# Kernel tuning notes

Hardware: AMD Instinct MI355X
Metric: run time of the kernel (lower is better)

Reference implementation:

```python
import jax, jax.numpy as jnp
import numpy as np

B, L, D, H = 2, 2048, 1024, 16
HD = D // H
SCALE = HD ** -0.5


def setup_inputs() -> dict:
    key = jax.random.key(0)
    ks = jax.random.split(key, 11)
    s = D ** -0.5  # torch Linear default init scale (uniform bound)
    return {
        "q": jax.random.normal(ks[0], (B, L, D), jnp.float32),
        "k": jax.random.normal(ks[1], (B, L, D), jnp.float32),
        "v": jax.random.normal(ks[2], (B, L, D), jnp.float32),
        "Wq": jax.random.uniform(ks[3], (D, D), jnp.float32, -s, s),
        "bq": jax.random.uniform(ks[4], (D,), jnp.float32, -s, s),
        "Wk": jax.random.uniform(ks[5], (D, D), jnp.float32, -s, s),
        "bk": jax.random.uniform(ks[6], (D,), jnp.float32, -s, s),
        "Wv": jax.random.uniform(ks[7], (D, D), jnp.float32, -s, s),
        "bv": jax.random.uniform(ks[8], (D,), jnp.float32, -s, s),
        "Wo": jax.random.uniform(ks[9], (D, D), jnp.float32, -s, s),
        "bo": jax.random.uniform(ks[10], (D,), jnp.float32, -s, s),
    }


def reference(q, k, v, Wq, bq, Wk, bk, Wv, bv, Wo, bo):
    b, q_len, _ = q.shape
    # projections; weights stored as (D, D) acting on the right: x @ W + b
    qh = (q @ Wq + bq).reshape(b, q_len, H, HD).transpose(0, 2, 1, 3)  # (B,H,Q,hd)
    kh = (k @ Wk + bk).reshape(b, -1, H, HD).transpose(0, 2, 1, 3)    # (B,H,K,hd)
    vh = (v @ Wv + bv).reshape(b, -1, H, HD).transpose(0, 2, 1, 3)    # (B,H,K,hd)
    att = jnp.einsum("bhqd,bhkd->bhqk", qh * SCALE, kh)               # (B,H,Q,K)
    att = jax.nn.softmax(att, axis=-1)
    out = jnp.einsum("bhqk,bhkd->bhqd", att, vh)                      # (B,H,Q,hd)
    out = out.transpose(0, 2, 1, 3).reshape(b, q_len, D)
    return out @ Wo + bo
```

## Files before the change

### kernel.cpp

```cpp
#include <hip/hip_runtime.h>

namespace {
constexpr int kB  = 2;
constexpr int kL  = 2048;
constexpr int kD  = 1024;
constexpr int kH  = 16;
constexpr int kHD = 64;
constexpr int kM  = kB * kL;
}

typedef _Float16 f16x8 __attribute__((ext_vector_type(8)));
typedef float    f32x16 __attribute__((ext_vector_type(16)));
typedef unsigned int u32;

union Frag16 { uint4 u4; unsigned u[4]; f16x8 v; };

__device__ __forceinline__ unsigned short f2h(float f) {
    return __builtin_bit_cast(unsigned short, (_Float16)f);
}
__device__ __forceinline__ unsigned pk2(float a, float b) {
    return __builtin_bit_cast(unsigned, __builtin_amdgcn_cvt_pkrtz(a, b));
}
__device__ __forceinline__ float max3f(float a, float b, float c) {
    float d;
    asm("v_max3_f32 %0, %1, %2, %3" : "=v"(d) : "v"(a), "v"(b), "v"(c));
    return d;
}

__device__ __forceinline__ void gload16(const void* g, void* l) {
    __builtin_amdgcn_global_load_lds(
        (const __attribute__((address_space(1))) u32*)g,
        (__attribute__((address_space(3))) u32*)(unsigned long long)(__builtin_bit_cast(unsigned long long, l)),
        16, 0, 0);
}

__global__ __launch_bounds__(256) void cast_f16_kernel(
    const float* __restrict__ q, const float* __restrict__ k,
    const float* __restrict__ v, unsigned short* __restrict__ dst)
{
    const float* src = blockIdx.y == 0 ? q : (blockIdx.y == 1 ? k : v);
    unsigned short* d = dst + (size_t)blockIdx.y * ((size_t)kM * kD);
    const size_t i = ((size_t)blockIdx.x * 256 + threadIdx.x) * 8;
    const float4 f0 = *(const float4*)(src + i);
    const float4 f1 = *(const float4*)(src + i + 4);
    _Float16 h[8];
    h[0] = (_Float16)f0.x; h[1] = (_Float16)f0.y;
    h[2] = (_Float16)f0.z; h[3] = (_Float16)f0.w;
    h[4] = (_Float16)f1.x; h[5] = (_Float16)f1.y;
    h[6] = (_Float16)f1.z; h[7] = (_Float16)f1.w;
    *(uint4*)(d + i) = *(uint4*)h;
}

__global__ __launch_bounds__(256) void tcast_kernel(
    const float* __restrict__ W0, const float* __restrict__ W1,
    const float* __restrict__ W2, const float* __restrict__ W3,
    unsigned short* __restrict__ WtBase)
{
    __shared__ _Float16 T[64][68];
    const float* W = blockIdx.z == 0 ? W0 : blockIdx.z == 1 ? W1
                   : blockIdx.z == 2 ? W2 : W3;
    unsigned short* Wt = WtBase + (size_t)blockIdx.z * ((size_t)kD * kD);
    const int k0 = blockIdx.y * 64, n0 = blockIdx.x * 64;
    const int tx = threadIdx.x & 15, ty = threadIdx.x >> 4;
#pragma unroll
    for (int i = 0; i < 4; ++i) {
        const int kk = i * 16 + ty;
        const float4 w = *(const float4*)&W[(size_t)(k0 + kk) * kD + n0 + tx * 4];
        T[tx * 4 + 0][kk] = (_Float16)w.x;
        T[tx * 4 + 1][kk] = (_Float16)w.y;
        T[tx * 4 + 2][kk] = (_Float16)w.z;
        T[tx * 4 + 3][kk] = (_Float16)w.w;
    }
    __syncthreads();
#pragma unroll
    for (int i = 0; i < 4; ++i) {
        const int nn = i * 16 + ty;
        *(ushort4*)&Wt[(size_t)(n0 + nn) * kD + k0 + tx * 4] = *(ushort4*)&T[nn][tx * 4];
    }
}

template <int MODE>
__global__ __launch_bounds__(256) void gemm16_kernel(
    const unsigned short* __restrict__ A, const unsigned short* __restrict__ Wt,
    const float* __restrict__ bias, void* __restrict__ Cv)
{
    __shared__ unsigned short Als[2][128 * 64];
    __shared__ unsigned short Bls[2][128 * 64];

    const int tid = threadIdx.x;
    const int lane = tid & 63;
    const int wid = tid >> 6;
    const int l31 = lane & 31;
    const int hi = lane >> 5;
    const int by = blockIdx.x & 31;
    const int bx = blockIdx.x >> 5;
    const int row0 = by * 128;
    const int col0 = bx * 128;
    const int wr = wid >> 1, wc = wid & 1;

    const int rl = lane >> 3;
    const int sl = lane & 7;
    const int ssrc = (sl ^ rl) * 8;

    const unsigned short* Abase = A + (size_t)(row0 + wid * 32 + rl) * kD + ssrc;
    const unsigned short* Bbase = Wt + (size_t)(col0 + wid * 32 + rl) * kD + ssrc;

    f32x16 acc00{}, acc01{}, acc10{}, acc11{};

    auto stage = [&](int kt, int buf) {
#pragma unroll
        for (int i = 0; i < 4; ++i) {
            gload16(Abase + (size_t)(i * 8) * kD + kt * 64,
                    &Als[buf][(wid * 32 + i * 8) * 64]);
        }
#pragma unroll
        for (int i = 0; i < 4; ++i) {
            gload16(Bbase + (size_t)(i * 8) * kD + kt * 64,
                    &Bls[buf][(wid * 32 + i * 8) * 64]);
        }
    };

    const int ra0 = wr * 64 + l31;
    const int cb0 = wc * 64 + l31;

    stage(0, 0);
    int cur = 0;
    for (int kt = 0; kt < kD / 64; ++kt) {
        __syncthreads();
        if (kt + 1 < kD / 64) stage(kt + 1, cur ^ 1);
#pragma unroll
        for (int ks = 0; ks < 4; ++ks) {
            const int slot = (ks << 1) | hi;
            Frag16 a0, a1, b0, b1;
            a0.u4 = *(const uint4*)&Als[cur][ra0 * 64 + ((slot ^ (ra0 & 7)) << 3)];
            a1.u4 = *(const uint4*)&Als[cur][(ra0 + 32) * 64 + ((slot ^ ((ra0 + 32) & 7)) << 3)];
            b0.u4 = *(const uint4*)&Bls[cur][cb0 * 64 + ((slot ^ (cb0 & 7)) << 3)];
            b1.u4 = *(const uint4*)&Bls[cur][(cb0 + 32) * 64 + ((slot ^ ((cb0 + 32) & 7)) << 3)];
            acc00 = __builtin_amdgcn_mfma_f32_32x32x16_f16(a0.v, b0.v, acc00, 0, 0, 0);
            acc01 = __builtin_amdgcn_mfma_f32_32x32x16_f16(a0.v, b1.v, acc01, 0, 0, 0);
            acc10 = __builtin_amdgcn_mfma_f32_32x32x16_f16(a1.v, b0.v, acc10, 0, 0, 0);
            acc11 = __builtin_amdgcn_mfma_f32_32x32x16_f16(a1.v, b1.v, acc11, 0, 0, 0);
        }
        cur ^= 1;
    }

    const float bias0 = bias[col0 + wc * 64 + l31];
    const float bias1 = bias[col0 + wc * 64 + 32 + l31];

    const f32x16* accs[2][2] = {{&acc00, &acc01}, {&acc10, &acc11}};
#pragma unroll
    for (int rt = 0; rt < 2; ++rt) {
#pragma unroll
        for (int ct = 0; ct < 2; ++ct) {
            const f32x16& acv = *accs[rt][ct];
            const float bb = ct ? bias1 : bias0;
            const int c = col0 + wc * 64 + ct * 32 + l31;
            if (MODE == 2) {
                unsigned short* C = (unsigned short*)Cv;
#pragma unroll
                for (int qd = 0; qd < 4; ++qd) {
                    const int r = row0 + wr * 64 + rt * 32 + 8 * qd + 4 * hi;
                    const int b_ = r >> 11, l_ = r & (kL - 1);
                    ushort4 w;
                    w.x = f2h(acv[4 * qd + 0] + bb);
                    w.y = f2h(acv[4 * qd + 1] + bb);
                    w.z = f2h(acv[4 * qd + 2] + bb);
                    w.w = f2h(acv[4 * qd + 3] + bb);
                    *(ushort4*)&C[((size_t)(b_ * kH + (c >> 6)) * kHD + (c & 63)) * kL + l_] = w;
                }
            } else {
#pragma unroll
                for (int reg = 0; reg < 16; ++reg) {
                    const int r = row0 + wr * 64 + rt * 32 + (reg & 3) + 8 * (reg >> 2) + 4 * hi;
                    const float val = acv[reg] + bb;
                    if (MODE == 0) {
                        ((float*)Cv)[(size_t)r * kD + c] = val;
                    } else {
                        const int b_ = r >> 11, l_ = r & (kL - 1);
                        ((unsigned short*)Cv)[((size_t)(b_ * kH + (c >> 6)) * kL + l_) * kHD + (c & 63)] = f2h(val);
                    }
                }
            }
        }
    }
}

__global__ __launch_bounds__(512) void attn_mfma_kernel(
    const unsigned short* __restrict__ Qh, const unsigned short* __restrict__ Kh,
    const unsigned short* __restrict__ Vt, unsigned short* __restrict__ Opart,
    float2* __restrict__ Stat)
{
    __shared__ unsigned short Kls[4][64 * 64];
    __shared__ unsigned short Vls[4][64 * 64];

    const int lane = threadIdx.x & 63;
    const int wid  = threadIdx.x >> 6;
    const int l31  = lane & 31;
    const int hi   = lane >> 5;

    const int id = blockIdx.x;
    const int j  = id >> 3;
    const int bh = (id & 7) * 4 + (j >> 4);
    const int qt = j & 7;
    const int ks = (j >> 3) & 1;
    const int q = qt * 256 + wid * 32 + l31;

    const size_t qkBase = (size_t)bh * kL * kHD;
    const unsigned short* Qp = Qh + qkBase + (size_t)q * kHD + hi * 8;
    Frag16 qf[4];
#pragma unroll
    for (int d = 0; d < 4; ++d) qf[d].u4 = *(const uint4*)(Qp + d * 16);

    const int srow = wid * 8 + (lane >> 3);
    const int soff = (((lane & 7) ^ (srow & 7)) << 3);
    const unsigned short* Kg = Kh + qkBase + (size_t)srow * kHD + soff;
    const unsigned short* Vg = Vt + (size_t)bh * kHD * kL + (size_t)srow * kL + soff;

    auto stage = [&](int kt, int buf) {
        gload16(Kg + (size_t)(kt * 64) * kHD, &Kls[buf][(wid * 8) * 64]);
        gload16(Vg + kt * 64,                 &Vls[buf][(wid * 8) * 64]);
    };

    f16x8 onesv;
#pragma unroll
    for (int i = 0; i < 8; ++i) onesv[i] = (_Float16)1.0f;

    f32x16 o0{}, o1{}, ls{};
    float m = -1e30f;
    const float cexp = 0.125f * 1.44269504089f;

    const int kt0 = ks * 16;
    stage(kt0 + 0, 0);
    stage(kt0 + 1, 1);

    for (int lt = 0; lt < 16; ++lt) {
        if (lt < 15) asm volatile("s_waitcnt vmcnt(2)" ::: "memory");
        else         asm volatile("s_waitcnt vmcnt(0)" ::: "memory");
        __builtin_amdgcn_s_barrier();
        if (lt + 2 < 16) stage(kt0 + lt + 2, (lt + 2) & 3);
        const int cur = lt & 3;

        const int rA = l31, rB = l31 + 32;
        f32x16 c0{}, c1{};
        Frag16 kf0[4], kf1[4];
#pragma unroll
        for (int d = 0; d < 4; ++d) {
            const int s = (d << 1) | hi;
            kf0[d].u4 = *(const uint4*)&Kls[cur][rA * 64 + ((s ^ (rA & 7)) << 3)];
            kf1[d].u4 = *(const uint4*)&Kls[cur][rB * 64 + ((s ^ (rB & 7)) << 3)];
        }
        Frag16 vf0[4], vf1[4];
#pragma unroll
        for (int ksl = 0; ksl < 4; ++ksl) {
            const int s = (ksl << 1) | hi;
            vf0[ksl].u4 = *(const uint4*)&Vls[cur][rA * 64 + ((s ^ (rA & 7)) << 3)];
            vf1[ksl].u4 = *(const uint4*)&Vls[cur][rB * 64 + ((s ^ (rB & 7)) << 3)];
        }
        __builtin_amdgcn_s_setprio(1);
#pragma unroll
        for (int d = 0; d < 4; ++d) {
            c0 = __builtin_amdgcn_mfma_f32_32x32x16_f16(kf0[d].v, qf[d].v, c0, 0, 0, 0);
            c1 = __builtin_amdgcn_mfma_f32_32x32x16_f16(kf1[d].v, qf[d].v, c1, 0, 0, 0);
        }
        __builtin_amdgcn_s_setprio(0);

        float mx = fmaxf(c0[0], c1[0]);
#pragma unroll
        for (int r = 1; r < 16; ++r) mx = max3f(mx, c0[r], c1[r]);
        mx = fmaxf(mx, __shfl_xor(mx, 32));
        if (mx > m + 48.f) {
            const float corr = __builtin_amdgcn_exp2f((m - mx) * cexp);
            m = mx;
            o0 *= corr;
            o1 *= corr;
            ls *= corr;
        }
        const float mc = m * cexp;

        unsigned u0[8], u1[8];
#pragma unroll
        for (int i = 0; i < 8; ++i) {
            u0[i] = pk2(__builtin_amdgcn_exp2f(fmaf(c0[2 * i], cexp, -mc)),
                        __builtin_amdgcn_exp2f(fmaf(c0[2 * i + 1], cexp, -mc)));
            u1[i] = pk2(__builtin_amdgcn_exp2f(fmaf(c1[2 * i], cexp, -mc)),
                        __builtin_amdgcn_exp2f(fmaf(c1[2 * i + 1], cexp, -mc)));
        }
        Frag16 pf[4];
        {
            unsigned t0 = hi ? u0[0] : u0[2];
            unsigned t1 = hi ? u0[1] : u0[3];
            unsigned t2 = hi ? u0[4] : u0[6];
            unsigned t3 = hi ? u0[5] : u0[7];
            const unsigned r0 = __shfl_xor(t0, 32);
            const unsigned r1 = __shfl_xor(t1, 32);
            const unsigned r2 = __shfl_xor(t2, 32);
            const unsigned r3 = __shfl_xor(t3, 32);
            pf[0].u[0] = hi ? r0 : u0[0];
            pf[0].u[1] = hi ? r1 : u0[1];
            pf[0].u[2] = hi ? u0[2] : r0;
            pf[0].u[3] = hi ? u0[3] : r1;
            pf[1].u[0] = hi ? r2 : u0[4];
            pf[1].u[1] = hi ? r3 : u0[5];
            pf[1].u[2] = hi ? u0[6] : r2;
            pf[1].u[3] = hi ? u0[7] : r3;
        }
        {
            unsigned t0 = hi ? u1[0] : u1[2];
            unsigned t1 = hi ? u1[1] : u1[3];
            unsigned t2 = hi ? u1[4] : u1[6];
            unsigned t3 = hi ? u1[5] : u1[7];
            const unsigned r0 = __shfl_xor(t0, 32);
            const unsigned r1 = __shfl_xor(t1, 32);
            const unsigned r2 = __shfl_xor(t2, 32);
            const unsigned r3 = __shfl_xor(t3, 32);
            pf[2].u[0] = hi ? r0 : u1[0];
            pf[2].u[1] = hi ? r1 : u1[1];
            pf[2].u[2] = hi ? u1[2] : r0;
            pf[2].u[3] = hi ? u1[3] : r1;
            pf[3].u[0] = hi ? r2 : u1[4];
            pf[3].u[1] = hi ? r3 : u1[5];
            pf[3].u[2] = hi ? u1[6] : r2;
            pf[3].u[3] = hi ? u1[7] : r3;
        }

        __builtin_amdgcn_s_setprio(1);
#pragma unroll
        for (int ksl = 0; ksl < 4; ++ksl) {
            o0 = __builtin_amdgcn_mfma_f32_32x32x16_f16(vf0[ksl].v, pf[ksl].v, o0, 0, 0, 0);
            o1 = __builtin_amdgcn_mfma_f32_32x32x16_f16(vf1[ksl].v, pf[ksl].v, o1, 0, 0, 0);
            ls = __builtin_amdgcn_mfma_f32_32x32x16_f16(onesv, pf[ksl].v, ls, 0, 0, 0);
        }
        __builtin_amdgcn_s_setprio(0);
    }

    const float lsum = ls[0];
    const size_t prow = (size_t)ks * (32 * kL) + (size_t)bh * kL + q;
    const float inv = 1.f / lsum;
    unsigned short* pp = Opart + prow * kHD;
#pragma unroll
    for (int g = 0; g < 4; ++g) {
        const int d = g * 8 + hi * 4;
        uint2 w0, w1;
        w0.x = pk2(o0[4 * g + 0] * inv, o0[4 * g + 1] * inv);
        w0.y = pk2(o0[4 * g + 2] * inv, o0[4 * g + 3] * inv);
        w1.x = pk2(o1[4 * g + 0] * inv, o1[4 * g + 1] * inv);
        w1.y = pk2(o1[4 * g + 2] * inv, o1[4 * g + 3] * inv);
        *(uint2*)(pp + d) = w0;
        *(uint2*)(pp + 32 + d) = w1;
    }
    if (hi == 0) Stat[prow] = make_float2(m, lsum);
}

__global__ __launch_bounds__(256) void merge_kernel(
    const unsigned short* __restrict__ Opart, const float2* __restrict__ Stat,
    unsigned short* __restrict__ O16)
{
    const int g = blockIdx.x * 256 + threadIdx.x;
    const int row = g >> 3;
    const int d0 = (g & 7) * 8;
    const int bh = row >> 11, q = row & (kL - 1);
    const float2 sa = Stat[row];
    const float2 sb = Stat[32 * kL + row];
    const float cexp = 0.125f * 1.44269504089f;
    const float M = fmaxf(sa.x, sb.x);
    float wa = __builtin_amdgcn_exp2f((sa.x - M) * cexp) * sa.y;
    float wb = __builtin_amdgcn_exp2f((sb.x - M) * cexp) * sb.y;
    const float inv = 1.f / (wa + wb);
    wa *= inv; wb *= inv;

    const unsigned short* pa = Opart + (size_t)row * kHD + d0;
    const unsigned short* pb = pa + (size_t)32 * kL * kHD;
    uint4 ua = *(const uint4*)pa;
    uint4 ub = *(const uint4*)pb;
    _Float16 ha[8], hb[8];
    *(uint4*)ha = ua;
    *(uint4*)hb = ub;
    unsigned out[4];
#pragma unroll
    for (int i = 0; i < 4; ++i) {
        const float v0 = wa * (float)ha[2 * i]     + wb * (float)hb[2 * i];
        const float v1 = wa * (float)ha[2 * i + 1] + wb * (float)hb[2 * i + 1];
        out[i] = pk2(v0, v1);
    }
    const int b_ = bh >> 4, h_ = bh & 15;
    *(uint4*)&O16[((size_t)(b_ * kL + q)) * kD + h_ * kHD + d0] = *(uint4*)out;
}

extern "C" void kernel_launch(void* const* d_in, const int* in_sizes, int n_in,
                              void* d_out, int out_size, void* d_ws, size_t ws_size,
                              hipStream_t stream)
{
    const float* q  = (const float*)d_in[0];
    const float* k  = (const float*)d_in[1];
    const float* v  = (const float*)d_in[2];
    const float* Wq = (const float*)d_in[3];
    const float* bq = (const float*)d_in[4];
    const float* Wk = (const float*)d_in[5];
    const float* bk = (const float*)d_in[6];
    const float* Wv = (const float*)d_in[7];
    const float* bv = (const float*)d_in[8];
    const float* Wo = (const float*)d_in[9];
    const float* bo = (const float*)d_in[10];
    float* out = (float*)d_out;

    const size_t MD = (size_t)kM * kD;
    const size_t DD = (size_t)kD * kD;
    unsigned short* A16 = (unsigned short*)d_ws;
    unsigned short* Wt16 = A16 + 3 * MD;
    unsigned short* Qh16 = Wt16 + 4 * DD;
    unsigned short* Kh16 = Qh16 + MD;
    unsigned short* Vt16 = Kh16 + MD;
    unsigned short* O16   = A16;
    unsigned short* Opart = A16 + MD;
    float2*         Stat  = (float2*)Wt16;

    const dim3 blk(256);

    hipLaunchKernelGGL(cast_f16_kernel, dim3(kM * kD / (256 * 8), 3), blk, 0, stream,
                       q, k, v, A16);
    hipLaunchKernelGGL(tcast_kernel, dim3(16, 16, 4), blk, 0, stream,
                       Wq, Wk, Wv, Wo, Wt16);

    hipLaunchKernelGGL((gemm16_kernel<1>), dim3(256), blk, 0, stream,
                       A16, Wt16, bq, (void*)Qh16);
    hipLaunchKernelGGL((gemm16_kernel<1>), dim3(256), blk, 0, stream,
                       A16 + MD, Wt16 + DD, bk, (void*)Kh16);
    hipLaunchKernelGGL((gemm16_kernel<2>), dim3(256), blk, 0, stream,
                       A16 + 2 * MD, Wt16 + 2 * DD, bv, (void*)Vt16);

    hipLaunchKernelGGL(attn_mfma_kernel, dim3(512), dim3(512), 0, stream,
                       Qh16, Kh16, Vt16, Opart, Stat);
    hipLaunchKernelGGL(merge_kernel, dim3(2048), blk, 0, stream,
                       Opart, Stat, O16);

    hipLaunchKernelGGL((gemm16_kernel<0>), dim3(256), blk, 0, stream,
                       O16, Wt16 + 3 * DD, bo, (void*)out);
}
```

Baseline: 142.7 us.

## Give each attention wave two query tiles and drop ones-MFMA row sum

The attention kernel now runs 4 waves per block instead of 8, and each wave handles 64 queries as two 32-query tiles. Each K and V fragment read from LDS therefore feeds twice as many MFMAs, halving LDS traffic per FLOP. Each wave also stages twice as many rows per tile. The softmax row sum is now accumulated with scalar adds plus a cross-half shuffle, replacing the extra MFMA against a ones vector. In exchange, accumulator register pressure roughly doubles, which can reduce occupancy, and there are half as many waves to hide latency.

Result: slower. 154.2 us (+8.0%).

```diff
diff --git a/kernel.cpp b/kernel.cpp
--- a/kernel.cpp
+++ b/kernel.cpp
@@ -185,7 +185,7 @@
     }
 }
 
-__global__ __launch_bounds__(512) void attn_mfma_kernel(
+__global__ __launch_bounds__(256) void attn_mfma_kernel(
     const unsigned short* __restrict__ Qh, const unsigned short* __restrict__ Kh,
     const unsigned short* __restrict__ Vt, unsigned short* __restrict__ Opart,
     float2* __restrict__ Stat)
@@ -201,154 +201,194 @@
     const int id = blockIdx.x;
     const int j  = id >> 3;
     const int bh = (id & 7) * 4 + (j >> 4);
-    const int qt = j & 7;
-    const int ks = (j >> 3) & 1;
-    const int q = qt * 256 + wid * 32 + l31;
+    const int rem = j & 15;
+    const int qt = rem & 7;
+    const int ks = rem >> 3;
+    const int qA = qt * 256 + wid * 64 + l31;
 
     const size_t qkBase = (size_t)bh * kL * kHD;
-    const unsigned short* Qp = Qh + qkBase + (size_t)q * kHD + hi * 8;
-    Frag16 qf[4];
-#pragma unroll
-    for (int d = 0; d < 4; ++d) qf[d].u4 = *(const uint4*)(Qp + d * 16);
-
-    const int srow = wid * 8 + (lane >> 3);
+    const unsigned short* QpA = Qh + qkBase + (size_t)qA * kHD + hi * 8;
+    Frag16 qfA[4], qfB[4];
+#pragma unroll
+    for (int d = 0; d < 4; ++d) {
+        qfA[d].u4 = *(const uint4*)(QpA + d * 16);
+        qfB[d].u4 = *(const uint4*)(QpA + (size_t)32 * kHD + d * 16);
+    }
+
+    const int srow = wid * 16 + (lane >> 3);
     const int soff = (((lane & 7) ^ (srow & 7)) << 3);
     const unsigned short* Kg = Kh + qkBase + (size_t)srow * kHD + soff;
     const unsigned short* Vg = Vt + (size_t)bh * kHD * kL + (size_t)srow * kL + soff;
 
     auto stage = [&](int kt, int buf) {
-        gload16(Kg + (size_t)(kt * 64) * kHD, &Kls[buf][(wid * 8) * 64]);
-        gload16(Vg + kt * 64,                 &Vls[buf][(wid * 8) * 64]);
+        gload16(Kg + (size_t)(kt * 64) * kHD,     &Kls[buf][(wid * 16) * 64]);
+        gload16(Kg + (size_t)(kt * 64 + 8) * kHD, &Kls[buf][(wid * 16 + 8) * 64]);
+        gload16(Vg + kt * 64,                     &Vls[buf][(wid * 16) * 64]);
+        gload16(Vg + kt * 64 + (size_t)8 * kL,    &Vls[buf][(wid * 16 + 8) * 64]);
     };
 
-    f16x8 onesv;
-#pragma unroll
-    for (int i = 0; i < 8; ++i) onesv[i] = (_Float16)1.0f;
-
-    f32x16 o0{}, o1{}, ls{};
-    float m = -1e30f;
+    auto buildpf = [&](const unsigned* u, Frag16* pf) {
+        unsigned t0 = hi ? u[0] : u[2];
+        unsigned t1 = hi ? u[1] : u[3];
+        unsigned t2 = hi ? u[4] : u[6];
+        unsigned t3 = hi ? u[5] : u[7];
+        const unsigned r0 = __shfl_xor(t0, 32);
+        const unsigned r1 = __shfl_xor(t1, 32);
+        const unsigned r2 = __shfl_xor(t2, 32);
+        const unsigned r3 = __shfl_xor(t3, 32);
+        pf[0].u[0] = hi ? r0 : u[0];
+        pf[0].u[1] = hi ? r1 : u[1];
+        pf[0].u[2] = hi ? u[2] : r0;
+        pf[0].u[3] = hi ? u[3] : r1;
+        pf[1].u[0] = hi ? r2 : u[4];
+        pf[1].u[1] = hi ? r3 : u[5];
+        pf[1].u[2] = hi ? u[6] : r2;
+        pf[1].u[3] = hi ? u[7] : r3;
+    };
+
+    f32x16 o00{}, o01{}, o10{}, o11{};
+    float m0 = -1e30f, m1 = -1e30f, ls0 = 0.f, ls1 = 0.f;
     const float cexp = 0.125f * 1.44269504089f;
+    const int rA = l31, rB = l31 + 32;
 
     const int kt0 = ks * 16;
     stage(kt0 + 0, 0);
     stage(kt0 + 1, 1);
 
     for (int lt = 0; lt < 16; ++lt) {
-        if (lt < 15) asm volatile("s_waitcnt vmcnt(2)" ::: "memory");
+        if (lt < 15) asm volatile("s_waitcnt vmcnt(4)" ::: "memory");
         else         asm volatile("s_waitcnt vmcnt(0)" ::: "memory");
         __builtin_amdgcn_s_barrier();
         if (lt + 2 < 16) stage(kt0 + lt + 2, (lt + 2) & 3);
         const int cur = lt & 3;
 
-        const int rA = l31, rB = l31 + 32;
-        f32x16 c0{}, c1{};
-        Frag16 kf0[4], kf1[4];
+        f32x16 c00{}, c01{}, c10{}, c11{};
+        __builtin_amdgcn_s_setprio(1);
 #pragma unroll
         for (int d = 0; d < 4; ++d) {
             const int s = (d << 1) | hi;
-            kf0[d].u4 = *(const uint4*)&Kls[cur][rA * 64 + ((s ^ (rA & 7)) << 3)];
-            kf1[d].u4 = *(const uint4*)&Kls[cur][rB * 64 + ((s ^ (rB & 7)) << 3)];
-        }
-        Frag16 vf0[4], vf1[4];
+            Frag16 k0, k1;
+            k0.u4 = *(const uint4*)&Kls[cur][rA * 64 + ((s ^ (rA & 7)) << 3)];
+            k1.u4 = *(const uint4*)&Kls[cur][rB * 64 + ((s ^ (rB & 7)) << 3)];
+            c00 = __builtin_amdgcn_mfma_f32_32x32x16_f16(k0.v, qfA[d].v, c00, 0, 0, 0);
+            c10 = __builtin_amdgcn_mfma_f32_32x32x16_f16(k0.v, qfB[d].v, c10, 0, 0, 0);
+            c01 = __builtin_amdgcn_mfma_f32_32x32x16_f16(k1.v, qfA[d].v, c01, 0, 0, 0);
+            c11 = __builtin_amdgcn_mfma_f32_32x32x16_f16(k1.v, qfB[d].v, c11, 0, 0, 0);
+        }
+        __builtin_amdgcn_s_setprio(0);
+
+        unsigned uA0[8], uA1[8], uB0[8], uB1[8];
+        {
+            float mx = fmaxf(c00[0], c01[0]);
+#pragma unroll
+            for (int r = 1; r < 16; ++r) mx = max3f(mx, c00[r], c01[r]);
+            mx = fmaxf(mx, __shfl_xor(mx, 32));
+            if (mx > m0 + 48.f) {
+                const float corr = __builtin_amdgcn_exp2f((m0 - mx) * cexp);
+                m0 = mx;
+                ls0 *= corr;
+                o00 *= corr;
+                o01 *= corr;
+            }
+            const float mc = m0 * cexp;
+            float rs = 0.f;
+#pragma unroll
+            for (int i = 0; i < 8; ++i) {
+                const float e0 = __builtin_amdgcn_exp2f(fmaf(c00[2 * i], cexp, -mc));
+                const float e1 = __builtin_amdgcn_exp2f(fmaf(c00[2 * i + 1], cexp, -mc));
+                const float e2 = __builtin_amdgcn_exp2f(fmaf(c01[2 * i], cexp, -mc));
+                const float e3 = __builtin_amdgcn_exp2f(fmaf(c01[2 * i + 1], cexp, -mc));
+                uA0[i] = pk2(e0, e1);
+                uA1[i] = pk2(e2, e3);
+                rs += (e0 + e1) + (e2 + e3);
+            }
+            rs += __shfl_xor(rs, 32);
+            ls0 += rs;
+        }
+        {
+            float mx = fmaxf(c10[0], c11[0]);
+#pragma unroll
+            for (int r = 1; r < 16; ++r) mx = max3f(mx, c10[r], c11[r]);
+            mx = fmaxf(mx, __shfl_xor(mx, 32));
+            if (mx > m1 + 48.f) {
+                const float corr = __builtin_amdgcn_exp2f((m1 - mx) * cexp);
+                m1 = mx;
+                ls1 *= corr;
+                o10 *= corr;
+                o11 *= corr;
+            }
+            const float mc = m1 * cexp;
+            float rs = 0.f;
+#pragma unroll
+            for (int i = 0; i < 8; ++i) {
+                const float e0 = __builtin_amdgcn_exp2f(fmaf(c10[2 * i], cexp, -mc));
+                const float e1 = __builtin_amdgcn_exp2f(fmaf(c10[2 * i + 1], cexp, -mc));
+                const float e2 = __builtin_amdgcn_exp2f(fmaf(c11[2 * i], cexp, -mc));
+                const float e3 = __builtin_amdgcn_exp2f(fmaf(c11[2 * i + 1], cexp, -mc));
+                uB0[i] = pk2(e0, e1);
+                uB1[i] = pk2(e2, e3);
+                rs += (e0 + e1) + (e2 + e3);
+            }
+            rs += __shfl_xor(rs, 32);
+            ls1 += rs;
+        }
+
+        Frag16 pfA[4], pfB[4];
+        buildpf(uA0, &pfA[0]);
+        buildpf(uA1, &pfA[2]);
+        buildpf(uB0, &pfB[0]);
+        buildpf(uB1, &pfB[2]);
+
+        __builtin_amdgcn_s_setprio(1);
 #pragma unroll
         for (int ksl = 0; ksl < 4; ++ksl) {
             const int s = (ksl << 1) | hi;
-            vf0[ksl].u4 = *(const uint4*)&Vls[cur][rA * 64 + ((s ^ (rA & 7)) << 3)];
-            vf1[ksl].u4 = *(const uint4*)&Vls[cur][rB * 64 + ((s ^ (rB & 7)) << 3)];
-        }
-        __builtin_amdgcn_s_setprio(1);
-#pragma unroll
-        for (int d = 0; d < 4; ++d) {
-            c0 = __builtin_amdgcn_mfma_f32_32x32x16_f16(kf0[d].v, qf[d].v, c0, 0, 0, 0);
-            c1 = __builtin_amdgcn_mfma_f32_32x32x16_f16(kf1[d].v, qf[d].v, c1, 0, 0, 0);
+            Frag16 v0, v1;
+            v0.u4 = *(const uint4*)&Vls[cur][rA * 64 + ((s ^ (rA & 7)) << 3)];
+            v1.u4 = *(const uint4*)&Vls[cur][rB * 64 + ((s ^ (rB & 7)) << 3)];
+            o00 = __builtin_amdgcn_mfma_f32_32x32x16_f16(v0.v, pfA[ksl].v, o00, 0, 0, 0);
+            o01 = __builtin_amdgcn_mfma_f32_32x32x16_f16(v1.v, pfA[ksl].v, o01, 0, 0, 0);
+            o10 = __builtin_amdgcn_mfma_f32_32x32x16_f16(v0.v, pfB[ksl].v, o10, 0, 0, 0);
+            o11 = __builtin_amdgcn_mfma_f32_32x32x16_f16(v1.v, pfB[ksl].v, o11, 0, 0, 0);
         }
         __builtin_amdgcn_s_setprio(0);
-
-        float mx = fmaxf(c0[0], c1[0]);
-#pragma unroll
-        for (int r = 1; r < 16; ++r) mx = max3f(mx, c0[r], c1[r]);
-        mx = fmaxf(mx, __shfl_xor(mx, 32));
-        if (mx > m + 48.f) {
-            const float corr = __builtin_amdgcn_exp2f((m - mx) * cexp);
-            m = mx;
-            o0 *= corr;
-            o1 *= corr;
-            ls *= corr;
-        }
-        const float mc = m * cexp;
-
-        unsigned u0[8], u1[8];
-#pragma unroll
-        for (int i = 0; i < 8; ++i) {
-            u0[i] = pk2(__builtin_amdgcn_exp2f(fmaf(c0[2 * i], cexp, -mc)),
-                        __builtin_amdgcn_exp2f(fmaf(c0[2 * i + 1], cexp, -mc)));
-            u1[i] = pk2(__builtin_amdgcn_exp2f(fmaf(c1[2 * i], cexp, -mc)),
-                        __builtin_amdgcn_exp2f(fmaf(c1[2 * i + 1], cexp, -mc)));
-        }
-        Frag16 pf[4];
-        {
-            unsigned t0 = hi ? u0[0] : u0[2];
-            unsigned t1 = hi ? u0[1] : u0[3];
-            unsigned t2 = hi ? u0[4] : u0[6];
-            unsigned t3 = hi ? u0[5] : u0[7];
-            const unsigned r0 = __shfl_xor(t0, 32);
-            const unsigned r1 = __shfl_xor(t1, 32);
-            const unsigned r2 = __shfl_xor(t2, 32);
-            const unsigned r3 = __shfl_xor(t3, 32);
-            pf[0].u[0] = hi ? r0 : u0[0];
-            pf[0].u[1] = hi ? r1 : u0[1];
-            pf[0].u[2] = hi ? u0[2] : r0;
-            pf[0].u[3] = hi ? u0[3] : r1;
-            pf[1].u[0] = hi ? r2 : u0[4];
-            pf[1].u[1] = hi ? r3 : u0[5];
-            pf[1].u[2] = hi ? u0[6] : r2;
-            pf[1].u[3] = hi ? u0[7] : r3;
-        }
-        {
-            unsigned t0 = hi ? u1[0] : u1[2];
-            unsigned t1 = hi ? u1[1] : u1[3];
-            unsigned t2 = hi ? u1[4] : u1[6];
-            unsigned t3 = hi ? u1[5] : u1[7];
-            const unsigned r0 = __shfl_xor(t0, 32);
-            const unsigned r1 = __shfl_xor(t1, 32);
-            const unsigned r2 = __shfl_xor(t2, 32);
-            const unsigned r3 = __shfl_xor(t3, 32);
-            pf[2].u[0] = hi ? r0 : u1[0];
-            pf[2].u[1] = hi ? r1 : u1[1];
-            pf[2].u[2] = hi ? u1[2] : r0;
-            pf[2].u[3] = hi ? u1[3] : r1;
-            pf[3].u[0] = hi ? r2 : u1[4];
-            pf[3].u[1] = hi ? r3 : u1[5];
-            pf[3].u[2] = hi ? u1[6] : r2;
-            pf[3].u[3] = hi ? u1[7] : r3;
-        }
-
-        __builtin_amdgcn_s_setprio(1);
-#pragma unroll
-        for (int ksl = 0; ksl < 4; ++ksl) {
-            o0 = __builtin_amdgcn_mfma_f32_32x32x16_f16(vf0[ksl].v, pf[ksl].v, o0, 0, 0, 0);
-            o1 = __builtin_amdgcn_mfma_f32_32x32x16_f16(vf1[ksl].v, pf[ksl].v, o1, 0, 0, 0);
-            ls = __builtin_amdgcn_mfma_f32_32x32x16_f16(onesv, pf[ksl].v, ls, 0, 0, 0);
-        }
-        __builtin_amdgcn_s_setprio(0);
-    }
-
-    const float lsum = ls[0];
-    const size_t prow = (size_t)ks * (32 * kL) + (size_t)bh * kL + q;
-    const float inv = 1.f / lsum;
-    unsigned short* pp = Opart + prow * kHD;
-#pragma unroll
-    for (int g = 0; g < 4; ++g) {
-        const int d = g * 8 + hi * 4;
-        uint2 w0, w1;
-        w0.x = pk2(o0[4 * g + 0] * inv, o0[4 * g + 1] * inv);
-        w0.y = pk2(o0[4 * g + 2] * inv, o0[4 * g + 3] * inv);
-        w1.x = pk2(o1[4 * g + 0] * inv, o1[4 * g + 1] * inv);
-        w1.y = pk2(o1[4 * g + 2] * inv, o1[4 * g + 3] * inv);
-        *(uint2*)(pp + d) = w0;
-        *(uint2*)(pp + 32 + d) = w1;
-    }
-    if (hi == 0) Stat[prow] = make_float2(m, lsum);
+    }
+
+    const size_t prowA = (size_t)ks * (32 * kL) + (size_t)bh * kL + qA;
+    {
+        const float inv = 1.f / ls0;
+        unsigned short* pp = Opart + prowA * kHD;
+#pragma unroll
+        for (int g = 0; g < 4; ++g) {
+            const int d = g * 8 + hi * 4;
+            uint2 w0, w1;
+            w0.x = pk2(o00[4 * g + 0] * inv, o00[4 * g + 1] * inv);
+            w0.y = pk2(o00[4 * g + 2] * inv, o00[4 * g + 3] * inv);
+            w1.x = pk2(o01[4 * g + 0] * inv, o01[4 * g + 1] * inv);
+            w1.y = pk2(o01[4 * g + 2] * inv, o01[4 * g + 3] * inv);
+            *(uint2*)(pp + d) = w0;
+            *(uint2*)(pp + 32 + d) = w1;
+        }
+    }
+    {
+        const float inv = 1.f / ls1;
+        unsigned short* pp = Opart + (prowA + 32) * kHD;
+#pragma unroll
+        for (int g = 0; g < 4; ++g) {
+            const int d = g * 8 + hi * 4;
+            uint2 w0, w1;
+            w0.x = pk2(o10[4 * g + 0] * inv, o10[4 * g + 1] * inv);
+            w0.y = pk2(o10[4 * g + 2] * inv, o10[4 * g + 3] * inv);
+            w1.x = pk2(o11[4 * g + 0] * inv, o11[4 * g + 1] * inv);
+            w1.y = pk2(o11[4 * g + 2] * inv, o11[4 * g + 3] * inv);
+            *(uint2*)(pp + d) = w0;
+            *(uint2*)(pp + 32 + d) = w1;
+        }
+    }
+    if (hi == 0) {
+        Stat[prowA] = make_float2(m0, ls0);
+        Stat[prowA + 32] = make_float2(m1, ls1);
+    }
 }
 
 __global__ __launch_bounds__(256) void merge_kernel(
@@ -428,7 +468,7 @@
     hipLaunchKernelGGL((gemm16_kernel<2>), dim3(256), blk, 0, stream,
                        A16 + 2 * MD, Wt16 + 2 * DD, bv, (void*)Vt16);
 
-    hipLaunchKernelGGL(attn_mfma_kernel, dim3(512), dim3(512), 0, stream,
+    hipLaunchKernelGGL(attn_mfma_kernel, dim3(512), blk, 0, stream,
                        Qh16, Kh16, Vt16, Opart, Stat);
     hipLaunchKernelGGL(merge_kernel, dim3(2048), blk, 0, stream,
                        Opart, Stat, O16);
```
